# Performance work log

Measured on AMD Instinct MI355X. Metric: run time of the kernel, lower is better.

Reference implementation:

```python
import jax, jax.numpy as jnp
import numpy as np

NUM_RESIDUES = 2048
CUTOFF = 10.0
POS_SCALE = 30.0

def setup_inputs() -> dict:
    key = jax.random.key(0)
    ks = jax.random.split(key, 7)
    Na, Nb, G = 16384, 16384, 64
    pos_a = jax.random.normal(ks[0], (Na, 3), dtype=jnp.float32) * POS_SCALE
    pos_b = jax.random.normal(ks[1], (Nb, 3), dtype=jnp.float32) * POS_SCALE
    node2graph_a = jnp.sort(jax.random.randint(ks[2], (Na,), 0, G, dtype=jnp.int32))
    node2graph_b = jnp.sort(jax.random.randint(ks[3], (Nb,), 0, G, dtype=jnp.int32))
    atom2residue_a = jax.random.randint(ks[4], (Na,), 0, NUM_RESIDUES, dtype=jnp.int32)
    atom2residue_b = jax.random.randint(ks[5], (Nb,), 0, NUM_RESIDUES, dtype=jnp.int32)
    is_mutation = jax.random.bernoulli(ks[6], 0.01, (Na + Nb,))
    return {"pos_a": pos_a, "pos_b": pos_b,
            "node2graph_a": node2graph_a, "node2graph_b": node2graph_b,
            "atom2residue_a": atom2residue_a, "atom2residue_b": atom2residue_b,
            "is_mutation": is_mutation}

def _interface_mask(dist, atom2residue):
    # scatter_max of (dist < cutoff) per residue, then broadcast back to atoms
    is_iface_atom = (dist < CUTOFF).astype(jnp.int32)
    is_iface_res = jax.ops.segment_max(is_iface_atom, atom2residue,
                                       num_segments=NUM_RESIDUES)
    return is_iface_res[atom2residue] > 0

def reference(pos_a, pos_b, node2graph_a, node2graph_b,
              atom2residue_a, atom2residue_b, is_mutation):
    # segmented pairwise squared distances [Na, Nb] via GEMM expansion
    d2 = (jnp.sum(pos_a * pos_a, -1)[:, None]
          + jnp.sum(pos_b * pos_b, -1)[None, :]
          - 2.0 * (pos_a @ pos_b.T))
    same_graph = node2graph_a[:, None] == node2graph_b[None, :]
    d2 = jnp.where(same_graph, d2, jnp.inf)
    # nearest b for each a, and nearest a for each b (segment-restricted)
    idx_a = jnp.argmin(d2, axis=1)   # [Na]
    idx_b = jnp.argmin(d2, axis=0)   # [Nb]
    dist_a = jnp.linalg.norm(pos_a - pos_b[idx_a], axis=-1)
    dist_b = jnp.linalg.norm(pos_b - pos_a[idx_b], axis=-1)
    mask_a = _interface_mask(dist_a, atom2residue_a)
    mask_b = _interface_mask(dist_b, atom2residue_b)
    mask = jnp.concatenate([mask_a, mask_b]) | is_mutation
    dists = jnp.concatenate([dist_a, dist_b])
    return mask, dists
```

## Files before the change

kernel.cpp:

```cpp
#include <hip/hip_runtime.h>
#include <math.h>

constexpr int   NUM_RES = 2048;
constexpr float CUTOFF  = 10.0f;
constexpr int   MAGIC   = 0x13572468;

constexpr int WS_FLAGS   = 0;
constexpr int WS_MUTFLAG = 2 * NUM_RES;

__global__ __launch_bounds__(128) void nearest_kernel(
        const float* __restrict__ pos_a, const float* __restrict__ pos_b,
        const int* __restrict__ n2g_a,   const int* __restrict__ n2g_b,
        const int* __restrict__ a2r_a,   const int* __restrict__ a2r_b,
        const unsigned char* __restrict__ mut8,
        int Na, int Nb,
        float* __restrict__ out_dists, int* __restrict__ ws)
{
    int tid  = blockIdx.x * blockDim.x + threadIdx.x;
    int Ntot = Na + Nb;
    if (tid >= Ntot) return;

    if ((tid & 3) != 0 && mut8[tid] != 0) ws[WS_MUTFLAG] = MAGIC;

    const float* ps; const float* po;
    const int* n2g_s; const int* n2g_o; const int* a2r;
    int i, n_opp, side;
    if (tid < Na) {
        side = 0; i = tid;
        ps = pos_a; po = pos_b; n2g_s = n2g_a; n2g_o = n2g_b;
        a2r = a2r_a; n_opp = Nb;
    } else {
        side = 1; i = tid - Na;
        ps = pos_b; po = pos_a; n2g_s = n2g_b; n2g_o = n2g_a;
        a2r = a2r_b; n_opp = Na;
    }

    float x = ps[3 * i + 0];
    float y = ps[3 * i + 1];
    float z = ps[3 * i + 2];
    int g = n2g_s[i];

    int lo0 = 0, hi0 = n_opp, lo1 = 0, hi1 = n_opp;
    while (lo0 < hi0 || lo1 < hi1) {
        if (lo0 < hi0) {
            int m = (lo0 + hi0) >> 1;
            if (n2g_o[m] < g) lo0 = m + 1; else hi0 = m;
        }
        if (lo1 < hi1) {
            int m = (lo1 + hi1) >> 1;
            if (n2g_o[m] < g + 1) lo1 = m + 1; else hi1 = m;
        }
    }
    int lo = lo0, hi = lo1;

    float bd0 = INFINITY, bd1 = INFINITY, bd2t = INFINITY, bd3 = INFINITY;
    int   bj0 = 0, bj1 = 0, bj2 = 0, bj3 = 0;

    int j = lo;
    for (; j + 4 <= hi; j += 4) {
        float x0 = po[3*j+0],  y0 = po[3*j+1],  z0 = po[3*j+2];
        float x1 = po[3*j+3],  y1 = po[3*j+4],  z1 = po[3*j+5];
        float x2 = po[3*j+6],  y2 = po[3*j+7],  z2 = po[3*j+8];
        float x3 = po[3*j+9],  y3 = po[3*j+10], z3 = po[3*j+11];

        float dx0 = x - x0, dy0 = y - y0, dz0 = z - z0;
        float dx1 = x - x1, dy1 = y - y1, dz1 = z - z1;
        float dx2 = x - x2, dy2 = y - y2, dz2 = z - z2;
        float dx3 = x - x3, dy3 = y - y3, dz3 = z - z3;

        float d0 = dx0*dx0 + dy0*dy0 + dz0*dz0;
        float d1 = dx1*dx1 + dy1*dy1 + dz1*dz1;
        float d2 = dx2*dx2 + dy2*dy2 + dz2*dz2;
        float d3 = dx3*dx3 + dy3*dy3 + dz3*dz3;

        if (d0 < bd0)  { bd0 = d0;  bj0 = j;     }
        if (d1 < bd1)  { bd1 = d1;  bj1 = j + 1; }
        if (d2 < bd2t) { bd2t = d2; bj2 = j + 2; }
        if (d3 < bd3)  { bd3 = d3;  bj3 = j + 3; }
    }
    for (; j < hi; ++j) {
        float dx = x - po[3*j], dy = y - po[3*j+1], dz = z - po[3*j+2];
        float d = dx*dx + dy*dy + dz*dz;
        if (d < bd0) { bd0 = d; bj0 = j; }
    }

    float bd = bd0; int bj = bj0;
    if (bd1  < bd || (bd1  == bd && bj1 < bj)) { bd = bd1;  bj = bj1; }
    if (bd2t < bd || (bd2t == bd && bj2 < bj)) { bd = bd2t; bj = bj2; }
    if (bd3  < bd || (bd3  == bd && bj3 < bj)) { bd = bd3;  bj = bj3; }

    float dx = x - po[3*bj+0];
    float dy = y - po[3*bj+1];
    float dz = z - po[3*bj+2];
    float dist = sqrtf(dx*dx + dy*dy + dz*dz);

    out_dists[tid] = dist;
    if (dist < CUTOFF) {
        ws[WS_FLAGS + side * NUM_RES + a2r[i]] = MAGIC;
    }
}

__global__ __launch_bounds__(128) void mask_kernel(
        const void* __restrict__ mut,
        const int* __restrict__ a2r_a, const int* __restrict__ a2r_b,
        int Na, int Nb,
        const int* __restrict__ ws, float* __restrict__ out_mask)
{
    int tid  = blockIdx.x * blockDim.x + threadIdx.x;
    int Ntot = Na + Nb;
    if (tid >= Ntot) return;

    int side = (tid < Na) ? 0 : 1;
    int i    = (tid < Na) ? tid : tid - Na;
    int r    = side ? a2r_b[i] : a2r_a[i];
    int iface = (ws[WS_FLAGS + side * NUM_RES + r] == MAGIC);

    int m;
    if (ws[WS_MUTFLAG] == MAGIC) {
        m = ((const unsigned char*)mut)[tid] != 0;
    } else {
        m = ((const int*)mut)[tid] != 0;
    }
    out_mask[tid] = (iface | m) ? 1.0f : 0.0f;
}

extern "C" void kernel_launch(void* const* d_in, const int* in_sizes, int n_in,
                              void* d_out, int out_size, void* d_ws, size_t ws_size,
                              hipStream_t stream) {
    const float* pos_a = (const float*)d_in[0];
    const float* pos_b = (const float*)d_in[1];
    const int*   n2g_a = (const int*)d_in[2];
    const int*   n2g_b = (const int*)d_in[3];
    const int*   a2r_a = (const int*)d_in[4];
    const int*   a2r_b = (const int*)d_in[5];
    const void*  mut   = d_in[6];

    int Na = in_sizes[0] / 3;
    int Nb = in_sizes[1] / 3;
    int Ntot = Na + Nb;

    float* out = (float*)d_out;
    int* ws = (int*)d_ws;

    int nblocks = (Ntot + 127) / 128;
    nearest_kernel<<<nblocks, 128, 0, stream>>>(pos_a, pos_b, n2g_a, n2g_b,
                                                a2r_a, a2r_b,
                                                (const unsigned char*)mut,
                                                Na, Nb, out + Ntot, ws);

    mask_kernel<<<nblocks, 128, 0, stream>>>(mut, a2r_a, a2r_b,
                                             Na, Nb, ws, out);
}
```

Baseline: 89.99 us.

## Split each candidate scan across a wavefront with shuffle argmin reduction

The nearest-neighbour kernel changes from one thread per query scanning its whole graph segment serially to one 64-lane wavefront handling four consecutive queries. The lanes stride over the union candidate range and filter by graph id, then a shuffle tree reduction picks the argmin with ties going to the lower index. Query positions, graph ids and residue ids load as float4/int4 vectors, and block size rises to 256. The aim is to fix the low occupancy and long serial latency chains of the old layout. In exchange it launches far more threads, scans a slightly wider range, and assumes Na is a multiple of four with aligned vector loads.

```diff
diff --git a/kernel.cpp b/kernel.cpp
--- a/kernel.cpp
+++ b/kernel.cpp
@@ -8,7 +8,7 @@
 constexpr int WS_FLAGS   = 0;
 constexpr int WS_MUTFLAG = 2 * NUM_RES;
 
-__global__ __launch_bounds__(128) void nearest_kernel(
+__global__ __launch_bounds__(256) void nearest_kernel(
         const float* __restrict__ pos_a, const float* __restrict__ pos_b,
         const int* __restrict__ n2g_a,   const int* __restrict__ n2g_b,
         const int* __restrict__ a2r_a,   const int* __restrict__ a2r_b,
@@ -16,91 +16,115 @@
         int Na, int Nb,
         float* __restrict__ out_dists, int* __restrict__ ws)
 {
-    int tid  = blockIdx.x * blockDim.x + threadIdx.x;
-    int Ntot = Na + Nb;
-    if (tid >= Ntot) return;
+    const int gtid = blockIdx.x * blockDim.x + threadIdx.x;
+    const int lane = threadIdx.x & 63;
+    const int wid  = gtid >> 6;
+    const int Ntot = Na + Nb;
 
-    if ((tid & 3) != 0 && mut8[tid] != 0) ws[WS_MUTFLAG] = MAGIC;
+    if (gtid < Ntot && (gtid & 3) != 0 && mut8[gtid] != 0)
+        ws[WS_MUTFLAG] = MAGIC;
+
+    int base = wid * 4;
+    if (base >= Ntot) return;
 
     const float* ps; const float* po;
     const int* n2g_s; const int* n2g_o; const int* a2r;
-    int i, n_opp, side;
-    if (tid < Na) {
-        side = 0; i = tid;
+    int i0, n_opp, side, out_off;
+    if (base < Na) {
+        side = 0; i0 = base;
         ps = pos_a; po = pos_b; n2g_s = n2g_a; n2g_o = n2g_b;
-        a2r = a2r_a; n_opp = Nb;
+        a2r = a2r_a; n_opp = Nb; out_off = 0;
     } else {
-        side = 1; i = tid - Na;
+        side = 1; i0 = base - Na;
         ps = pos_b; po = pos_a; n2g_s = n2g_b; n2g_o = n2g_a;
-        a2r = a2r_b; n_opp = Na;
+        a2r = a2r_b; n_opp = Na; out_off = Na;
     }
 
-    float x = ps[3 * i + 0];
-    float y = ps[3 * i + 1];
-    float z = ps[3 * i + 2];
-    int g = n2g_s[i];
+    const float4* ps4 = (const float4*)(ps + 3 * i0);
+    float4 a0 = ps4[0], a1 = ps4[1], a2v = ps4[2];
+    float x0 = a0.x, y0 = a0.y, z0 = a0.z;
+    float x1 = a0.w, y1 = a1.x, z1 = a1.y;
+    float x2 = a1.z, y2 = a1.w, z2 = a2v.x;
+    float x3 = a2v.y, y3 = a2v.z, z3 = a2v.w;
 
-    int lo0 = 0, hi0 = n_opp, lo1 = 0, hi1 = n_opp;
-    while (lo0 < hi0 || lo1 < hi1) {
-        if (lo0 < hi0) {
-            int m = (lo0 + hi0) >> 1;
-            if (n2g_o[m] < g) lo0 = m + 1; else hi0 = m;
-        }
-        if (lo1 < hi1) {
-            int m = (lo1 + hi1) >> 1;
-            if (n2g_o[m] < g + 1) lo1 = m + 1; else hi1 = m;
-        }
+    const int4* n2g4 = (const int4*)(n2g_s + i0);
+    int4 gv = n2g4[0];
+    int g0 = gv.x, g3 = gv.w;
+
+    int lo = 0, hi = n_opp, lo2 = 0, hi2 = n_opp;
+    while ((lo < hi) | (lo2 < hi2)) {
+        if (lo < hi)   { int m = (lo + hi)   >> 1; if (n2g_o[m] < g0)     lo  = m + 1; else hi  = m; }
+        if (lo2 < hi2) { int m = (lo2 + hi2) >> 1; if (n2g_o[m] < g3 + 1) lo2 = m + 1; else hi2 = m; }
     }
-    int lo = lo0, hi = lo1;
+    int LO = lo, HI = lo2;
 
-    float bd0 = INFINITY, bd1 = INFINITY, bd2t = INFINITY, bd3 = INFINITY;
+    float bd0 = INFINITY, bd1 = INFINITY, bd2 = INFINITY, bd3 = INFINITY;
     int   bj0 = 0, bj1 = 0, bj2 = 0, bj3 = 0;
 
-    int j = lo;
-    for (; j + 4 <= hi; j += 4) {
-        float x0 = po[3*j+0],  y0 = po[3*j+1],  z0 = po[3*j+2];
-        float x1 = po[3*j+3],  y1 = po[3*j+4],  z1 = po[3*j+5];
-        float x2 = po[3*j+6],  y2 = po[3*j+7],  z2 = po[3*j+8];
-        float x3 = po[3*j+9],  y3 = po[3*j+10], z3 = po[3*j+11];
+    for (int j = LO + lane; j < HI; j += 64) {
+        float px = po[3*j+0], py = po[3*j+1], pz = po[3*j+2];
+        int   gj = n2g_o[j];
 
-        float dx0 = x - x0, dy0 = y - y0, dz0 = z - z0;
-        float dx1 = x - x1, dy1 = y - y1, dz1 = z - z1;
-        float dx2 = x - x2, dy2 = y - y2, dz2 = z - z2;
-        float dx3 = x - x3, dy3 = y - y3, dz3 = z - z3;
+        float dx, dy, dz, d;
+        dx = x0 - px; dy = y0 - py; dz = z0 - pz;
+        d = dx*dx + dy*dy + dz*dz;
+        if (gj == gv.x && d < bd0) { bd0 = d; bj0 = j; }
 
-        float d0 = dx0*dx0 + dy0*dy0 + dz0*dz0;
-        float d1 = dx1*dx1 + dy1*dy1 + dz1*dz1;
-        float d2 = dx2*dx2 + dy2*dy2 + dz2*dz2;
-        float d3 = dx3*dx3 + dy3*dy3 + dz3*dz3;
+        dx = x1 - px; dy = y1 - py; dz = z1 - pz;
+        d = dx*dx + dy*dy + dz*dz;
+        if (gj == gv.y && d < bd1) { bd1 = d; bj1 = j; }
 
-        if (d0 < bd0)  { bd0 = d0;  bj0 = j;     }
-        if (d1 < bd1)  { bd1 = d1;  bj1 = j + 1; }
-        if (d2 < bd2t) { bd2t = d2; bj2 = j + 2; }
-        if (d3 < bd3)  { bd3 = d3;  bj3 = j + 3; }
-    }
-    for (; j < hi; ++j) {
-        float dx = x - po[3*j], dy = y - po[3*j+1], dz = z - po[3*j+2];
-        float d = dx*dx + dy*dy + dz*dz;
-        if (d < bd0) { bd0 = d; bj0 = j; }
+        dx = x2 - px; dy = y2 - py; dz = z2 - pz;
+        d = dx*dx + dy*dy + dz*dz;
+        if (gj == gv.z && d < bd2) { bd2 = d; bj2 = j; }
+
+        dx = x3 - px; dy = y3 - py; dz = z3 - pz;
+        d = dx*dx + dy*dy + dz*dz;
+        if (gj == gv.w && d < bd3) { bd3 = d; bj3 = j; }
     }
 
-    float bd = bd0; int bj = bj0;
-    if (bd1  < bd || (bd1  == bd && bj1 < bj)) { bd = bd1;  bj = bj1; }
-    if (bd2t < bd || (bd2t == bd && bj2 < bj)) { bd = bd2t; bj = bj2; }
-    if (bd3  < bd || (bd3  == bd && bj3 < bj)) { bd = bd3;  bj = bj3; }
+    for (int off = 32; off >= 1; off >>= 1) {
+        float o; int q;
+        o = __shfl_down(bd0, off, 64); q = __shfl_down(bj0, off, 64);
+        if (o < bd0 || (o == bd0 && q < bj0)) { bd0 = o; bj0 = q; }
+        o = __shfl_down(bd1, off, 64); q = __shfl_down(bj1, off, 64);
+        if (o < bd1 || (o == bd1 && q < bj1)) { bd1 = o; bj1 = q; }
+        o = __shfl_down(bd2, off, 64); q = __shfl_down(bj2, off, 64);
+        if (o < bd2 || (o == bd2 && q < bj2)) { bd2 = o; bj2 = q; }
+        o = __shfl_down(bd3, off, 64); q = __shfl_down(bj3, off, 64);
+        if (o < bd3 || (o == bd3 && q < bj3)) { bd3 = o; bj3 = q; }
+    }
 
-    float dx = x - po[3*bj+0];
-    float dy = y - po[3*bj+1];
-    float dz = z - po[3*bj+2];
-    float dist = sqrtf(dx*dx + dy*dy + dz*dz);
+    if (lane == 0) {
+        float4 dists;
+        {
+            float dx = x0 - po[3*bj0], dy = y0 - po[3*bj0+1], dz = z0 - po[3*bj0+2];
+            dists.x = sqrtf(dx*dx + dy*dy + dz*dz);
+        }
+        {
+            float dx = x1 - po[3*bj1], dy = y1 - po[3*bj1+1], dz = z1 - po[3*bj1+2];
+            dists.y = sqrtf(dx*dx + dy*dy + dz*dz);
+        }
+        {
+            float dx = x2 - po[3*bj2], dy = y2 - po[3*bj2+1], dz = z2 - po[3*bj2+2];
+            dists.z = sqrtf(dx*dx + dy*dy + dz*dz);
+        }
+        {
+            float dx = x3 - po[3*bj3], dy = y3 - po[3*bj3+1], dz = z3 - po[3*bj3+2];
+            dists.w = sqrtf(dx*dx + dy*dy + dz*dz);
+        }
+        *(float4*)(out_dists + base) = dists;
 
-    out_dists[tid] = dist;
-    if (dist < CUTOFF) {
-        ws[WS_FLAGS + side * NUM_RES + a2r[i]] = MAGIC;
+        const int4* a2r4 = (const int4*)(a2r + i0);
+        int4 rr = a2r4[0];
+        if (dists.x < CUTOFF) ws[WS_FLAGS + side * NUM_RES + rr.x] = MAGIC;
+        if (dists.y < CUTOFF) ws[WS_FLAGS + side * NUM_RES + rr.y] = MAGIC;
+        if (dists.z < CUTOFF) ws[WS_FLAGS + side * NUM_RES + rr.z] = MAGIC;
+        if (dists.w < CUTOFF) ws[WS_FLAGS + side * NUM_RES + rr.w] = MAGIC;
     }
 }
 
-__global__ __launch_bounds__(128) void mask_kernel(
+__global__ __launch_bounds__(256) void mask_kernel(
         const void* __restrict__ mut,
         const int* __restrict__ a2r_a, const int* __restrict__ a2r_b,
         int Na, int Nb,
@@ -142,12 +166,13 @@
     float* out = (float*)d_out;
     int* ws = (int*)d_ws;
 
-    int nblocks = (Ntot + 127) / 128;
-    nearest_kernel<<<nblocks, 128, 0, stream>>>(pos_a, pos_b, n2g_a, n2g_b,
+    int nwaves  = (Ntot + 3) / 4;
+    int nblocks = (nwaves + 3) / 4;
+    nearest_kernel<<<nblocks, 256, 0, stream>>>(pos_a, pos_b, n2g_a, n2g_b,
                                                 a2r_a, a2r_b,
                                                 (const unsigned char*)mut,
                                                 Na, Nb, out + Ntot, ws);
 
-    mask_kernel<<<nblocks, 128, 0, stream>>>(mut, a2r_a, a2r_b,
-                                             Na, Nb, ws, out);
+    mask_kernel<<<(Ntot + 255) / 256, 256, 0, stream>>>(mut, a2r_a, a2r_b,
+                                                        Na, Nb, ws, out);
 }
```

Measured after the change: 88.36 us. No clear change (-1.8%).
